# Optimization experiments

Hardware: AMD Instinct MI355X
Metric: run time of the kernel (lower is better)

## Reference

```python
import jax, jax.numpy as jnp
import numpy as np

N, E, F_IN, HID, HEADS, OUT, G = 50000, 800000, 128, 64, 4, 10, 64
NEG_SLOPE = 0.2


def _glorot(key, shape):
    fan = shape[0] + shape[-1]
    lim = np.sqrt(6.0 / fan)
    return jax.random.uniform(key, shape, jnp.float32, -lim, lim)


def setup_inputs() -> dict:
    key = jax.random.key(0)
    ks = jax.random.split(key, 20)
    x = jax.random.normal(ks[0], (N, F_IN), jnp.float32)
    edge_index = jax.random.randint(ks[1], (2, E), 0, N, jnp.int64)
    batch = jnp.sort(jax.random.randint(ks[2], (N,), 0, G, jnp.int64))
    inp = {"x": x, "edge_index": edge_index, "batch": batch}
    # layer 1: in=F_IN, heads=HEADS, out=HID
    inp["W1"] = _glorot(ks[3], (F_IN, HEADS * HID))
    inp["b1"] = jnp.zeros((HEADS * HID,), jnp.float32)
    inp["as1"] = _glorot(ks[4], (HEADS, HID))
    inp["ad1"] = _glorot(ks[5], (HEADS, HID))
    # layer 2: in=HEADS*HID, heads=HEADS, out=HID
    inp["W2"] = _glorot(ks[6], (HEADS * HID, HEADS * HID))
    inp["b2"] = jnp.zeros((HEADS * HID,), jnp.float32)
    inp["as2"] = _glorot(ks[7], (HEADS, HID))
    inp["ad2"] = _glorot(ks[8], (HEADS, HID))
    # layer 3: in=HEADS*HID, heads=1, out=HID
    inp["W3"] = _glorot(ks[9], (HEADS * HID, HID))
    inp["b3"] = jnp.zeros((HID,), jnp.float32)
    inp["as3"] = _glorot(ks[10], (1, HID))
    inp["ad3"] = _glorot(ks[11], (1, HID))
    # MLP head [HID, HID, OUT]
    inp["Wm1"] = _glorot(ks[12], (HID, HID))
    inp["bm1"] = jnp.zeros((HID,), jnp.float32)
    inp["Wm2"] = _glorot(ks[13], (HID, OUT))
    inp["bm2"] = jnp.zeros((OUT,), jnp.float32)
    return inp


def _gat_layer(x, src, dst, W, b, att_src, att_dst):
    # x: [N, Fin]; att_*: [H, C]
    H, C = att_src.shape
    h = (x @ W).reshape(N, H, C)
    a_src = jnp.einsum("nhc,hc->nh", h, att_src)
    a_dst = jnp.einsum("nhc,hc->nh", h, att_dst)
    alpha = jax.nn.leaky_relu(a_src[src] + a_dst[dst], NEG_SLOPE)  # [E', H]
    amax = jax.ops.segment_max(alpha, dst, num_segments=N)
    alpha = jnp.exp(alpha - amax[dst])
    denom = jax.ops.segment_sum(alpha, dst, num_segments=N)
    alpha = alpha / (denom[dst] + 1e-16)
    msg = h[src] * alpha[:, :, None]  # [E', H, C]
    out = jax.ops.segment_sum(msg, dst, num_segments=N)  # [N, H, C]
    return out.reshape(N, H * C) + b


def reference(x, edge_index, batch, W1, b1, as1, ad1, W2, b2, as2, ad2, W3, b3, as3, ad3, Wm1, bm1, Wm2, bm2):
    # PyG GATConv adds self-loops by default
    loops = jnp.arange(N, dtype=edge_index.dtype)
    src = jnp.concatenate([edge_index[0], loops])
    dst = jnp.concatenate([edge_index[1], loops])
    h = jax.nn.relu(_gat_layer(x, src, dst, W1, b1, as1, ad1))
    h = jax.nn.relu(_gat_layer(h, src, dst, W2, b2, as2, ad2))
    h = jax.nn.relu(_gat_layer(h, src, dst, W3, b3, as3, ad3))
    pooled = jax.ops.segment_sum(h, batch, num_segments=G)  # [G, HID]
    hidden = jax.nn.relu(pooled @ Wm1 + bm1)
    return hidden @ Wm2 + bm2
```

## Files before the change

### kernel.cpp

```cpp
#include <hip/hip_runtime.h>
#include <hip/hip_bf16.h>

#define F_IN   128
#define HID    64
#define HEADS  4
#define OUTD   10
#define NGRP   64

typedef unsigned short u16;
typedef __attribute__((ext_vector_type(8))) short short8;
typedef __attribute__((ext_vector_type(4))) float f32x4;

__device__ __forceinline__ float atomAddF(float* p, float v) {
    return __hip_atomic_fetch_add(p, v, __ATOMIC_RELAXED, __HIP_MEMORY_SCOPE_AGENT);
}
__device__ __forceinline__ float lrelu(float f) { return f > 0.f ? f : 0.2f * f; }
__device__ __forceinline__ float b2f(u16 u) { return __uint_as_float(((unsigned)u) << 16); }
__device__ __forceinline__ u16 f2b(float f) {
    unsigned u = __float_as_uint(f);
    return (u16)((u + 0x7fffu + ((u >> 16) & 1u)) >> 16);
}
__device__ __forceinline__ unsigned fmono(float f) {
    unsigned u = __float_as_uint(f);
    return (u & 0x80000000u) ? ~u : (u | 0x80000000u);
}
__device__ __forceinline__ float funmono(unsigned u) {
    return __uint_as_float((u & 0x80000000u) ? (u & 0x7FFFFFFFu) : ~u);
}

__global__ __launch_bounds__(256) void wtrans_all_kernel(const float* __restrict__ W1,
                                                         const float* __restrict__ W2,
                                                         const float* __restrict__ W3,
                                                         u16* __restrict__ Wt1,
                                                         u16* __restrict__ Wt2,
                                                         u16* __restrict__ Wt3) {
    int i = blockIdx.x * 256 + threadIdx.x;
    if (i < 32768) {
        int n = i >> 7, k = i & 127;
        Wt1[i] = f2b(W1[(size_t)k * 256 + n]);
    } else if (i < 98304) {
        int j = i - 32768;
        int n = j >> 8, k = j & 255;
        Wt2[j] = f2b(W2[(size_t)k * 256 + n]);
    } else if (i < 114688) {
        int j = i - 98304;
        int n = j >> 8, k = j & 255;
        Wt3[j] = f2b(W3[(size_t)k * 64 + n]);
    }
}

template<int K, int NC, bool AF32>
__global__ __launch_bounds__(512) void gemm_att_kernel(const void* __restrict__ Aptr,
                                                       const u16* __restrict__ Bt,
                                                       const float* __restrict__ as_,
                                                       const float* __restrict__ ad_,
                                                       u16* __restrict__ Hb,
                                                       float* __restrict__ a_src,
                                                       float* __restrict__ a_dst,
                                                       int nrows) {
    constexpr int LDA = 40;
    constexpr int HH = NC / 64;
    __shared__ u16 As[128][LDA];
    __shared__ u16 Bs[NC][LDA];
    int tid = threadIdx.x;
    int m0 = blockIdx.x * 128;
    int w = tid >> 6, l = tid & 63, lr = l & 15, lk = l >> 4;

    if constexpr (NC == 256) {
        int wr = w >> 2, wc = w & 3;
        f32x4 acc[4][4] = {};
        for (int k0 = 0; k0 < K; k0 += 32) {
            {
                int row = tid >> 2, ks = (tid & 3) * 8;
                int grow = m0 + row;
                short8 av = {};
                if (grow < nrows) {
                    if constexpr (AF32) {
                        const float* src = (const float*)Aptr + (size_t)grow * K + k0 + ks;
                        float4 v0 = *(const float4*)src;
                        float4 v1 = *(const float4*)(src + 4);
                        av[0] = (short)f2b(v0.x); av[1] = (short)f2b(v0.y);
                        av[2] = (short)f2b(v0.z); av[3] = (short)f2b(v0.w);
                        av[4] = (short)f2b(v1.x); av[5] = (short)f2b(v1.y);
                        av[6] = (short)f2b(v1.z); av[7] = (short)f2b(v1.w);
                    } else {
                        av = *(const short8*)&((const u16*)Aptr)[(size_t)grow * K + k0 + ks];
                    }
                }
                *(short8*)&As[row][ks] = av;
            }
            #pragma unroll
            for (int i = 0; i < 2; i++) {
                int col = (tid >> 2) + 128 * i;
                int ks = (tid & 3) * 8;
                *(short8*)&Bs[col][ks] = *(const short8*)&Bt[(size_t)col * K + k0 + ks];
            }
            __syncthreads();
            short8 a[4], b[4];
            #pragma unroll
            for (int mi = 0; mi < 4; mi++) a[mi] = *(const short8*)&As[64 * wr + 16 * mi + lr][lk * 8];
            #pragma unroll
            for (int ni = 0; ni < 4; ni++) b[ni] = *(const short8*)&Bs[64 * wc + 16 * ni + lr][lk * 8];
            #pragma unroll
            for (int mi = 0; mi < 4; mi++)
                #pragma unroll
                for (int ni = 0; ni < 4; ni++)
                    acc[mi][ni] = __builtin_amdgcn_mfma_f32_16x16x32_bf16(a[mi], b[ni], acc[mi][ni], 0, 0, 0);
            __syncthreads();
        }
        #pragma unroll
        for (int mi = 0; mi < 4; mi++) {
            #pragma unroll
            for (int j = 0; j < 4; j++) {
                int grow = m0 + 64 * wr + 16 * mi + lk * 4 + j;
                if (grow < nrows) {
                    #pragma unroll
                    for (int ni = 0; ni < 4; ni++)
                        Hb[(size_t)grow * NC + 64 * wc + 16 * ni + lr] = f2b(acc[mi][ni][j]);
                }
            }
        }
        float asv[4], adv[4];
        #pragma unroll
        for (int ni = 0; ni < 4; ni++) {
            asv[ni] = as_[wc * 64 + 16 * ni + lr];
            adv[ni] = ad_[wc * 64 + 16 * ni + lr];
        }
        #pragma unroll
        for (int mi = 0; mi < 4; mi++) {
            #pragma unroll
            for (int j = 0; j < 4; j++) {
                float ps = 0.f, pd = 0.f;
                #pragma unroll
                for (int ni = 0; ni < 4; ni++) {
                    float v = acc[mi][ni][j];
                    ps += v * asv[ni];
                    pd += v * adv[ni];
                }
                #pragma unroll
                for (int o = 1; o < 16; o <<= 1) {
                    ps += __shfl_xor(ps, o, 64);
                    pd += __shfl_xor(pd, o, 64);
                }
                int grow = m0 + 64 * wr + 16 * mi + lk * 4 + j;
                if (lr == 0 && grow < nrows) {
                    a_src[grow * HH + wc] = ps;
                    a_dst[grow * HH + wc] = pd;
                }
            }
        }
    } else {
        f32x4 acc[4] = {};
        for (int k0 = 0; k0 < K; k0 += 32) {
            {
                int row = tid >> 2, ks = (tid & 3) * 8;
                int grow = m0 + row;
                short8 av = {};
                if (grow < nrows) av = *(const short8*)&((const u16*)Aptr)[(size_t)grow * K + k0 + ks];
                *(short8*)&As[row][ks] = av;
            }
            if (tid < 256) {
                int col = tid >> 2;
                int ks = (tid & 3) * 8;
                *(short8*)&Bs[col][ks] = *(const short8*)&Bt[(size_t)col * K + k0 + ks];
            }
            __syncthreads();
            short8 af = *(const short8*)&As[16 * w + lr][lk * 8];
            #pragma unroll
            for (int c = 0; c < 4; c++) {
                short8 bf = *(const short8*)&Bs[c * 16 + lr][lk * 8];
                acc[c] = __builtin_amdgcn_mfma_f32_16x16x32_bf16(af, bf, acc[c], 0, 0, 0);
            }
            __syncthreads();
        }
        #pragma unroll
        for (int c = 0; c < 4; c++) {
            #pragma unroll
            for (int j = 0; j < 4; j++) {
                int grow = m0 + 16 * w + lk * 4 + j;
                if (grow < nrows) Hb[(size_t)grow * NC + c * 16 + lr] = f2b(acc[c][j]);
            }
        }
        float asv[4], adv[4];
        #pragma unroll
        for (int c = 0; c < 4; c++) {
            asv[c] = as_[c * 16 + lr];
            adv[c] = ad_[c * 16 + lr];
        }
        #pragma unroll
        for (int j = 0; j < 4; j++) {
            float ps = 0.f, pd = 0.f;
            #pragma unroll
            for (int c = 0; c < 4; c++) {
                float v = acc[c][j];
                ps += v * asv[c];
                pd += v * adv[c];
            }
            #pragma unroll
            for (int o = 1; o < 16; o <<= 1) {
                ps += __shfl_xor(ps, o, 64);
                pd += __shfl_xor(pd, o, 64);
            }
            int grow = m0 + 16 * w + lk * 4 + j;
            if (lr == 0 && grow < nrows) {
                a_src[grow] = ps;
                a_dst[grow] = pd;
            }
        }
    }
}

template<int HH>
__global__ __launch_bounds__(256) void gmax_kernel(const float* __restrict__ a_src,
                                                   unsigned* __restrict__ gmaxu, int n_nodes) {
    float mx[HH];
    #pragma unroll
    for (int h = 0; h < HH; h++) mx[h] = -3.4e38f;
    for (int i = blockIdx.x * 256 + threadIdx.x; i < n_nodes; i += gridDim.x * 256) {
        #pragma unroll
        for (int h = 0; h < HH; h++) mx[h] = fmaxf(mx[h], a_src[i * HH + h]);
    }
    #pragma unroll
    for (int h = 0; h < HH; h++) {
        #pragma unroll
        for (int off = 32; off; off >>= 1) mx[h] = fmaxf(mx[h], __shfl_xor(mx[h], off, 64));
    }
    if ((threadIdx.x & 63) == 0) {
        #pragma unroll
        for (int h = 0; h < HH; h++) atomicMax(&gmaxu[h], fmono(mx[h]));
    }
}

__global__ void count_kernel(const int* __restrict__ ei, int* __restrict__ deg,
                             int E_, int n_nodes) {
    int e = blockIdx.x * 256 + threadIdx.x;
    int tot = E_ + n_nodes;
    if (e >= tot) return;
    int d = (e < E_) ? ei[E_ + e] : e - E_;
    atomicAdd(&deg[d], 1);
}

__global__ __launch_bounds__(256) void scan_reduce_kernel(const int* __restrict__ deg,
                                                          int* __restrict__ bsum, int n) {
    int i = blockIdx.x * 256 + threadIdx.x;
    int v = (i < n) ? deg[i] : 0;
    #pragma unroll
    for (int o = 32; o; o >>= 1) v += __shfl_xor(v, o, 64);
    __shared__ int ws[4];
    if ((threadIdx.x & 63) == 0) ws[threadIdx.x >> 6] = v;
    __syncthreads();
    if (threadIdx.x == 0) bsum[blockIdx.x] = ws[0] + ws[1] + ws[2] + ws[3];
}

__global__ __launch_bounds__(256) void scan_blocksums_kernel(int* __restrict__ bsum, int nb) {
    __shared__ int s[256];
    int t = threadIdx.x;
    int v = (t < nb) ? bsum[t] : 0;
    s[t] = v;
    __syncthreads();
    #pragma unroll
    for (int d = 1; d < 256; d <<= 1) {
        int x = (t >= d) ? s[t - d] : 0;
        __syncthreads();
        s[t] += x;
        __syncthreads();
    }
    if (t < nb) bsum[t] = s[t] - v;
}

__global__ __launch_bounds__(256) void scan_final_kernel(const int* __restrict__ deg,
                                                         const int* __restrict__ bsum,
                                                         int* __restrict__ off, int n) {
    __shared__ int s[256];
    int t = threadIdx.x;
    int i = blockIdx.x * 256 + t;
    int v = (i < n) ? deg[i] : 0;
    s[t] = v;
    __syncthreads();
    #pragma unroll
    for (int d = 1; d < 256; d <<= 1) {
        int x = (t >= d) ? s[t - d] : 0;
        __syncthreads();
        s[t] += x;
        __syncthreads();
    }
    int ex = s[t] - v + bsum[blockIdx.x];
    if (i < n) off[i] = ex;
    if (i == n - 1) off[n] = ex + v;
}

__global__ void fill_kernel(const int* __restrict__ ei, const int* __restrict__ off,
                            int* __restrict__ cursor, int* __restrict__ csr_src,
                            int E_, int n_nodes) {
    int e = blockIdx.x * 256 + threadIdx.x;
    int tot = E_ + n_nodes;
    if (e >= tot) return;
    int s, d;
    if (e < E_) { s = ei[e]; d = ei[E_ + e]; } else { s = d = e - E_; }
    int pos = atomicAdd(&cursor[d], 1);
    csr_src[off[d] + pos] = s;
}

__global__ __launch_bounds__(256) void gat_aggr_kernel(const int* __restrict__ off,
                                                       const int* __restrict__ csr_src,
                                                       const u16* __restrict__ Hb,
                                                       const float* __restrict__ a_src,
                                                       const float* __restrict__ a_dst,
                                                       const unsigned* __restrict__ gmaxu,
                                                       const float* __restrict__ bias,
                                                       u16* __restrict__ outb16,
                                                       int d_base, int n_hi) {
    constexpr int HH = 4, HC = 256, GRP = 16;
    int d = d_base + blockIdx.x * 4 + (threadIdx.x >> 6);
    if (d >= n_hi) return;
    int lane = threadIdx.x & 63;
    int hh = lane >> 4;
    int g = lane & 15;
    int gb = lane & 48;
    int o0 = off[d];
    int deg = off[d + 1] - o0;
    float adm = a_dst[d * HH + hh];
    float m = lrelu(funmono(gmaxu[hh]) + adm);

    float den = 0.f;
    float acc[4] = {};
    int j = 0;
    for (; j + 4 <= deg; j += 4) {
        int s0 = csr_src[o0 + j + 0];
        int s1 = csr_src[o0 + j + 1];
        int s2 = csr_src[o0 + j + 2];
        int s3 = csr_src[o0 + j + 3];
        int ssel = s3;
        if (g == 0) ssel = s0; else if (g == 1) ssel = s1; else if (g == 2) ssel = s2;
        float e = __expf(lrelu(a_src[ssel * HH + hh] + adm) - m);
        float e0 = __shfl(e, gb + 0, 64);
        float e1 = __shfl(e, gb + 1, 64);
        float e2 = __shfl(e, gb + 2, 64);
        float e3 = __shfl(e, gb + 3, 64);
        den += (e0 + e1) + (e2 + e3);
        uint2 h0 = *(const uint2*)&Hb[(size_t)s0 * HC + lane * 4];
        uint2 h1 = *(const uint2*)&Hb[(size_t)s1 * HC + lane * 4];
        uint2 h2 = *(const uint2*)&Hb[(size_t)s2 * HC + lane * 4];
        uint2 h3 = *(const uint2*)&Hb[(size_t)s3 * HC + lane * 4];
        acc[0] += e0 * __uint_as_float(h0.x << 16) + e1 * __uint_as_float(h1.x << 16)
                + e2 * __uint_as_float(h2.x << 16) + e3 * __uint_as_float(h3.x << 16);
        acc[1] += e0 * __uint_as_float(h0.x & 0xffff0000u) + e1 * __uint_as_float(h1.x & 0xffff0000u)
                + e2 * __uint_as_float(h2.x & 0xffff0000u) + e3 * __uint_as_float(h3.x & 0xffff0000u);
        acc[2] += e0 * __uint_as_float(h0.y << 16) + e1 * __uint_as_float(h1.y << 16)
                + e2 * __uint_as_float(h2.y << 16) + e3 * __uint_as_float(h3.y << 16);
        acc[3] += e0 * __uint_as_float(h0.y & 0xffff0000u) + e1 * __uint_as_float(h1.y & 0xffff0000u)
                + e2 * __uint_as_float(h2.y & 0xffff0000u) + e3 * __uint_as_float(h3.y & 0xffff0000u);
    }
    for (; j < deg; j++) {
        int s = csr_src[o0 + j];
        float al = __expf(lrelu(a_src[s * HH + hh] + adm) - m);
        den += al;
        uint2 hv = *(const uint2*)&Hb[(size_t)s * HC + lane * 4];
        acc[0] += al * __uint_as_float(hv.x << 16);
        acc[1] += al * __uint_as_float(hv.x & 0xffff0000u);
        acc[2] += al * __uint_as_float(hv.y << 16);
        acc[3] += al * __uint_as_float(hv.y & 0xffff0000u);
    }
    float inv = 1.f / (den + 1e-16f);
    float4 bv = *(const float4*)&bias[lane * 4];
    float v0 = fmaxf(acc[0] * inv + bv.x, 0.f);
    float v1 = fmaxf(acc[1] * inv + bv.y, 0.f);
    float v2 = fmaxf(acc[2] * inv + bv.z, 0.f);
    float v3 = fmaxf(acc[3] * inv + bv.w, 0.f);
    uint2 o;
    o.x = (unsigned)f2b(v0) | ((unsigned)f2b(v1) << 16);
    o.y = (unsigned)f2b(v2) | ((unsigned)f2b(v3) << 16);
    *(uint2*)&outb16[(size_t)d * HC + lane * 4] = o;
}

__global__ __launch_bounds__(256) void gat_aggr3_kernel(const int* __restrict__ off,
                                                        const int* __restrict__ csr_src,
                                                        const u16* __restrict__ Hb,
                                                        const float* __restrict__ a_src,
                                                        const float* __restrict__ a_dst,
                                                        const unsigned* __restrict__ gmaxu,
                                                        const float* __restrict__ bias,
                                                        float* __restrict__ outf32,
                                                        int n_nodes) {
    int d = blockIdx.x * 4 + (threadIdx.x >> 6);
    if (d >= n_nodes) return;
    int lane = threadIdx.x & 63;
    int grp = lane >> 4;
    int li = lane & 15;
    int o0 = off[d];
    int deg = off[d + 1] - o0;
    float adm = a_dst[d];
    float m = lrelu(funmono(gmaxu[0]) + adm);

    float den = 0.f;
    float a0 = 0.f, a1 = 0.f, a2 = 0.f, a3 = 0.f;
    for (int j = 0; j < deg; j += 4) {
        int e = j + grp;
        float al = 0.f;
        unsigned hx = 0u, hy = 0u;
        if (e < deg) {
            int s = csr_src[o0 + e];
            al = __expf(lrelu(a_src[s] + adm) - m);
            uint2 hv = *(const uint2*)&Hb[(size_t)s * 64 + li * 4];
            hx = hv.x; hy = hv.y;
        }
        den += al;
        a0 += al * __uint_as_float(hx << 16);
        a1 += al * __uint_as_float(hx & 0xffff0000u);
        a2 += al * __uint_as_float(hy << 16);
        a3 += al * __uint_as_float(hy & 0xffff0000u);
    }
    #pragma unroll
    for (int o = 16; o < 64; o <<= 1) {
        den += __shfl_xor(den, o, 64);
        a0  += __shfl_xor(a0, o, 64);
        a1  += __shfl_xor(a1, o, 64);
        a2  += __shfl_xor(a2, o, 64);
        a3  += __shfl_xor(a3, o, 64);
    }
    if (grp == 0) {
        float inv = 1.f / (den + 1e-16f);
        float4 bv = *(const float4*)&bias[li * 4];
        float4 o;
        o.x = fmaxf(a0 * inv + bv.x, 0.f);
        o.y = fmaxf(a1 * inv + bv.y, 0.f);
        o.z = fmaxf(a2 * inv + bv.z, 0.f);
        o.w = fmaxf(a3 * inv + bv.w, 0.f);
        *(float4*)&outf32[(size_t)d * 64 + li * 4] = o;
    }
}

__global__ __launch_bounds__(256) void pool_kernel(const float* __restrict__ H3,
                                                   const int* __restrict__ batch,
                                                   float* __restrict__ pooled, int n_nodes) {
    int wave = (blockIdx.x * 256 + threadIdx.x) >> 6;
    int lane = threadIdx.x & 63;
    int nwaves = gridDim.x * 4;
    int chunk = (n_nodes + nwaves - 1) / nwaves;
    int start = wave * chunk;
    int end = min(n_nodes, start + chunk);
    if (start >= end) return;
    int cur = batch[start];
    float acc = 0.f;
    for (int n = start; n < end; n++) {
        int g = batch[n];
        if (g != cur) { atomAddF(&pooled[cur * 64 + lane], acc); acc = 0.f; cur = g; }
        acc += H3[(size_t)n * 64 + lane];
    }
    atomAddF(&pooled[cur * 64 + lane], acc);
}

__global__ __launch_bounds__(64) void mlp_kernel(const float* __restrict__ pooled,
                                                 const float* __restrict__ Wm1,
                                                 const float* __restrict__ bm1,
                                                 const float* __restrict__ Wm2,
                                                 const float* __restrict__ bm2,
                                                 float* __restrict__ out) {
    __shared__ float sp[64], sh[64];
    int g = blockIdx.x, t = threadIdx.x;
    sp[t] = pooled[g * 64 + t];
    __syncthreads();
    float a = bm1[t];
    for (int k = 0; k < 64; k++) a += sp[k] * Wm1[k * 64 + t];
    sh[t] = a > 0.f ? a : 0.f;
    __syncthreads();
    if (t < 10) {
        float o = bm2[t];
        for (int j = 0; j < 64; j++) o += sh[j] * Wm2[j * 10 + t];
        out[g * 10 + t] = o;
    }
}

extern "C" void kernel_launch(void* const* d_in, const int* in_sizes, int n_in,
                              void* d_out, int out_size, void* d_ws, size_t ws_size,
                              hipStream_t stream) {
    const float* x   = (const float*)d_in[0];
    const int*   ei  = (const int*)d_in[1];
    const int*   bat = (const int*)d_in[2];
    const float* W1  = (const float*)d_in[3];
    const float* b1  = (const float*)d_in[4];
    const float* as1 = (const float*)d_in[5];
    const float* ad1 = (const float*)d_in[6];
    const float* W2  = (const float*)d_in[7];
    const float* b2  = (const float*)d_in[8];
    const float* as2 = (const float*)d_in[9];
    const float* ad2 = (const float*)d_in[10];
    const float* W3  = (const float*)d_in[11];
    const float* b3  = (const float*)d_in[12];
    const float* as3 = (const float*)d_in[13];
    const float* ad3 = (const float*)d_in[14];
    const float* Wm1 = (const float*)d_in[15];
    const float* bm1 = (const float*)d_in[16];
    const float* Wm2 = (const float*)d_in[17];
    const float* bm2 = (const float*)d_in[18];
    float* out = (float*)d_out;

    const int Nn = in_sizes[0] / F_IN;
    const int Ee = in_sizes[1] / 2;
    const int Et = Ee + Nn;

    char* wsp = (char*)d_ws;
    size_t off_b = 0;
    auto alloc = [&](size_t bytes) { void* p = wsp + off_b; off_b += (bytes + 255) & ~(size_t)255; return p; };
    u16*   HbA     = (u16*)alloc((size_t)Nn * 256 * 2);
    u16*   HbB     = (u16*)alloc((size_t)Nn * 256 * 2);
    float* Hf      = (float*)alloc((size_t)Nn * HID * 4);
    u16*   Wt1     = (u16*)alloc((size_t)256 * 128 * 2);
    u16*   Wt2     = (u16*)alloc((size_t)256 * 256 * 2);
    u16*   Wt3     = (u16*)alloc((size_t)64 * 256 * 2);
    float* a_src   = (float*)alloc((size_t)Nn * HEADS * 4);
    float* a_dst   = (float*)alloc((size_t)Nn * HEADS * 4);
    size_t zcount = 16 + (size_t)Nn * 2 + NGRP * HID;
    unsigned* zbase = (unsigned*)alloc(zcount * 4);
    unsigned* gmaxu = zbase;
    int*   deg     = (int*)(zbase + 16);
    int*   cursor  = deg + Nn;
    float* pooled  = (float*)(cursor + Nn);
    int*   bsum    = (int*)alloc((size_t)256 * 4);
    int*   csr_off = (int*)alloc((size_t)(Nn + 1) * 4);
    int*   csr_src = (int*)alloc((size_t)Et * 4);
    (void)ws_size;

    wtrans_all_kernel<<<(114688 + 255) / 256, 256, 0, stream>>>(W1, W2, W3, Wt1, Wt2, Wt3);

    hipMemsetAsync(zbase, 0, zcount * 4, stream);

    int eb = (Et + 255) / 256;
    int nb = (Nn + 255) / 256;
    count_kernel<<<eb, 256, 0, stream>>>(ei, deg, Ee, Nn);
    scan_reduce_kernel<<<nb, 256, 0, stream>>>(deg, bsum, Nn);
    scan_blocksums_kernel<<<1, 256, 0, stream>>>(bsum, nb);
    scan_final_kernel<<<nb, 256, 0, stream>>>(deg, bsum, csr_off, Nn);
    fill_kernel<<<eb, 256, 0, stream>>>(ei, csr_off, cursor, csr_src, Ee, Nn);

    const int gemm_blocks = (Nn + 127) / 128;
    const int nodeBlocks = (Nn + 3) / 4;
    const int half = (Nn + 1) / 2;
    const int halfBlocks = (half + 3) / 4;

    auto run_big_aggr = [&](const u16* Hsrc, const unsigned* gm, const float* b, u16* dst) {
        gat_aggr_kernel<<<halfBlocks, 256, 0, stream>>>(csr_off, csr_src, Hsrc,
                                                        a_src, a_dst, gm, b, dst, 0, half);
        gat_aggr_kernel<<<halfBlocks, 256, 0, stream>>>(csr_off, csr_src, Hsrc,
                                                        a_src, a_dst, gm, b, dst, half, Nn);
    };

    gemm_att_kernel<128, 256, true><<<gemm_blocks, 512, 0, stream>>>(x, Wt1, as1, ad1,
                                                                     HbA, a_src, a_dst, Nn);
    gmax_kernel<4><<<64, 256, 0, stream>>>(a_src, gmaxu + 0, Nn);
    run_big_aggr(HbA, gmaxu + 0, b1, HbB);
    gemm_att_kernel<256, 256, false><<<gemm_blocks, 512, 0, stream>>>(HbB, Wt2, as2, ad2,
                                                                      HbA, a_src, a_dst, Nn);
    gmax_kernel<4><<<64, 256, 0, stream>>>(a_src, gmaxu + 4, Nn);
    run_big_aggr(HbA, gmaxu + 4, b2, HbB);
    gemm_att_kernel<256, 64, false><<<gemm_blocks, 512, 0, stream>>>(HbB, Wt3, as3, ad3,
                                                                     HbA, a_src, a_dst, Nn);
    gmax_kernel<1><<<64, 256, 0, stream>>>(a_src, gmaxu + 8, Nn);
    gat_aggr3_kernel<<<nodeBlocks, 256, 0, stream>>>(csr_off, csr_src, HbA,
                                                     a_src, a_dst, gmaxu + 8, b3, Hf, Nn);

    pool_kernel<<<128, 256, 0, stream>>>(Hf, bat, pooled, Nn);
    mlp_kernel<<<NGRP, 64, 0, stream>>>(pooled, Wm1, bm1, Wm2, bm2, out);
}
```

Measured before the change: 413.3 us.

## Partition CSR fill by destination range, merge aggr launches, unroll layer-3 gather

The CSR fill is split into four launches, each scattering only edges whose destination falls in one quarter of the node range. This is meant to keep atomics and csr_src writes local to a smaller region and more cache-friendly, at the cost of reading the edge list four times. The two half-range aggregation launches per big layer are merged into one full launch. The layer-3 aggregation loop gains an 8-edge unrolled body that issues two gathers per lane to raise memory-level parallelism.

After: 395.9 us. 1.04x faster.

```diff
diff --git a/kernel.cpp b/kernel.cpp
--- a/kernel.cpp
+++ b/kernel.cpp
@@ -289,14 +289,15 @@
     if (i == n - 1) off[n] = ex + v;
 }
 
-__global__ void fill_kernel(const int* __restrict__ ei, const int* __restrict__ off,
-                            int* __restrict__ cursor, int* __restrict__ csr_src,
-                            int E_, int n_nodes) {
+__global__ void fill_part_kernel(const int* __restrict__ ei, const int* __restrict__ off,
+                                 int* __restrict__ cursor, int* __restrict__ csr_src,
+                                 int E_, int n_nodes, int d_lo, int d_hi) {
     int e = blockIdx.x * 256 + threadIdx.x;
     int tot = E_ + n_nodes;
     if (e >= tot) return;
     int s, d;
     if (e < E_) { s = ei[e]; d = ei[E_ + e]; } else { s = d = e - E_; }
+    if (d < d_lo || d >= d_hi) return;
     int pos = atomicAdd(&cursor[d], 1);
     csr_src[off[d] + pos] = s;
 }
@@ -309,10 +310,10 @@
                                                        const unsigned* __restrict__ gmaxu,
                                                        const float* __restrict__ bias,
                                                        u16* __restrict__ outb16,
-                                                       int d_base, int n_hi) {
-    constexpr int HH = 4, HC = 256, GRP = 16;
-    int d = d_base + blockIdx.x * 4 + (threadIdx.x >> 6);
-    if (d >= n_hi) return;
+                                                       int n_nodes) {
+    constexpr int HH = 4, HC = 256;
+    int d = blockIdx.x * 4 + (threadIdx.x >> 6);
+    if (d >= n_nodes) return;
     int lane = threadIdx.x & 63;
     int hh = lane >> 4;
     int g = lane & 15;
@@ -394,7 +395,21 @@
 
     float den = 0.f;
     float a0 = 0.f, a1 = 0.f, a2 = 0.f, a3 = 0.f;
-    for (int j = 0; j < deg; j += 4) {
+    int j = 0;
+    for (; j + 8 <= deg; j += 8) {
+        int sA = csr_src[o0 + j + grp];
+        int sB = csr_src[o0 + j + 4 + grp];
+        float alA = __expf(lrelu(a_src[sA] + adm) - m);
+        float alB = __expf(lrelu(a_src[sB] + adm) - m);
+        uint2 hA = *(const uint2*)&Hb[(size_t)sA * 64 + li * 4];
+        uint2 hB = *(const uint2*)&Hb[(size_t)sB * 64 + li * 4];
+        den += alA + alB;
+        a0 += alA * __uint_as_float(hA.x << 16) + alB * __uint_as_float(hB.x << 16);
+        a1 += alA * __uint_as_float(hA.x & 0xffff0000u) + alB * __uint_as_float(hB.x & 0xffff0000u);
+        a2 += alA * __uint_as_float(hA.y << 16) + alB * __uint_as_float(hB.y << 16);
+        a3 += alA * __uint_as_float(hA.y & 0xffff0000u) + alB * __uint_as_float(hB.y & 0xffff0000u);
+    }
+    for (; j < deg; j += 4) {
         int e = j + grp;
         float al = 0.f;
         unsigned hx = 0u, hy = 0u;
@@ -531,28 +546,28 @@
     scan_reduce_kernel<<<nb, 256, 0, stream>>>(deg, bsum, Nn);
     scan_blocksums_kernel<<<1, 256, 0, stream>>>(bsum, nb);
     scan_final_kernel<<<nb, 256, 0, stream>>>(deg, bsum, csr_off, Nn);
-    fill_kernel<<<eb, 256, 0, stream>>>(ei, csr_off, cursor, csr_src, Ee, Nn);
+    {
+        int q = (Nn + 3) / 4;
+        for (int p = 0; p < 4; p++) {
+            int lo = p * q, hi = min(Nn, lo + q);
+            fill_part_kernel<<<eb, 256, 0, stream>>>(ei, csr_off, cursor, csr_src,
+                                                     Ee, Nn, lo, hi);
+        }
+    }
 
     const int gemm_blocks = (Nn + 127) / 128;
     const int nodeBlocks = (Nn + 3) / 4;
-    const int half = (Nn + 1) / 2;
-    const int halfBlocks = (half + 3) / 4;
-
-    auto run_big_aggr = [&](const u16* Hsrc, const unsigned* gm, const float* b, u16* dst) {
-        gat_aggr_kernel<<<halfBlocks, 256, 0, stream>>>(csr_off, csr_src, Hsrc,
-                                                        a_src, a_dst, gm, b, dst, 0, half);
-        gat_aggr_kernel<<<halfBlocks, 256, 0, stream>>>(csr_off, csr_src, Hsrc,
-                                                        a_src, a_dst, gm, b, dst, half, Nn);
-    };
 
     gemm_att_kernel<128, 256, true><<<gemm_blocks, 512, 0, stream>>>(x, Wt1, as1, ad1,
                                                                      HbA, a_src, a_dst, Nn);
     gmax_kernel<4><<<64, 256, 0, stream>>>(a_src, gmaxu + 0, Nn);
-    run_big_aggr(HbA, gmaxu + 0, b1, HbB);
+    gat_aggr_kernel<<<nodeBlocks, 256, 0, stream>>>(csr_off, csr_src, HbA,
+                                                    a_src, a_dst, gmaxu + 0, b1, HbB, Nn);
     gemm_att_kernel<256, 256, false><<<gemm_blocks, 512, 0, stream>>>(HbB, Wt2, as2, ad2,
                                                                       HbA, a_src, a_dst, Nn);
     gmax_kernel<4><<<64, 256, 0, stream>>>(a_src, gmaxu + 4, Nn);
-    run_big_aggr(HbA, gmaxu + 4, b2, HbB);
+    gat_aggr_kernel<<<nodeBlocks, 256, 0, stream>>>(csr_off, csr_src, HbA,
+                                                    a_src, a_dst, gmaxu + 4, b2, HbB, Nn);
     gemm_att_kernel<256, 64, false><<<gemm_blocks, 512, 0, stream>>>(HbB, Wt3, as3, ad3,
                                                                      HbA, a_src, a_dst, Nn);
     gmax_kernel<1><<<64, 256, 0, stream>>>(a_src, gmaxu + 8, Nn);
```
